# Kernel optimization log

Measured on AMD Instinct MI355X. Metric: run time of the kernel, lower is better.

Reference implementation:

```python
import jax, jax.numpy as jnp
import numpy as np

N_NODES = 100000
N_EDGES = 1600000
F_IN = 128
HID = 64
EPS = 1e-5


def setup_inputs() -> dict:
    key = jax.random.key(0)
    ks = jax.random.split(key, 16)
    x = jax.random.normal(ks[0], (N_NODES, F_IN), dtype=jnp.float32)
    edge_index = jax.random.randint(ks[1], (2, N_EDGES), 0, N_NODES, dtype=jnp.int64)
    inp = {"x": x, "edge_index": edge_index}
    # GCN layers: layer 0 maps F_IN->HID, layers 1,2 map HID->HID
    dims = [(F_IN, HID), (HID, HID), (HID, HID)]
    for i, (fi, fo) in enumerate(dims):
        inp[f"W{i}"] = jax.random.normal(ks[2 + i], (fi, fo), dtype=jnp.float32) / np.sqrt(fi)
        inp[f"b{i}"] = jnp.zeros((fo,), dtype=jnp.float32)
        inp[f"g{i}"] = jnp.ones((fo,), dtype=jnp.float32)
        inp[f"bt{i}"] = jnp.zeros((fo,), dtype=jnp.float32)
    inp["lw1"] = jax.random.normal(ks[8], (HID, HID // 2), dtype=jnp.float32) / np.sqrt(HID)
    inp["lb1"] = jnp.zeros((HID // 2,), dtype=jnp.float32)
    inp["lw2"] = jax.random.normal(ks[9], (HID // 2, 1), dtype=jnp.float32) / np.sqrt(HID // 2)
    inp["lb2"] = jnp.zeros((1,), dtype=jnp.float32)
    return inp


def _gcn_norm(edge_index, n_nodes):
    # add self loops, symmetric normalization D^{-1/2}(A+I)D^{-1/2}
    loops = jnp.arange(n_nodes, dtype=edge_index.dtype)
    src = jnp.concatenate([edge_index[0], loops])
    dst = jnp.concatenate([edge_index[1], loops])
    deg = jax.ops.segment_sum(jnp.ones_like(dst, dtype=jnp.float32), dst, num_segments=n_nodes)
    dinv = jax.lax.rsqrt(deg)  # deg >= 1 thanks to self loops
    norm = dinv[src] * dinv[dst]  # [E+N]
    return src, dst, norm


def reference(x, edge_index, W0, b0, g0, bt0, W1, b1, g1, bt1, W2, b2, g2, bt2, lw1, lb1, lw2, lb2):
    n = x.shape[0]
    src, dst, norm = _gcn_norm(edge_index, n)
    layers = [(W0, b0, g0, bt0), (W1, b1, g1, bt1), (W2, b2, g2, bt2)]
    h = x
    for W, b, g, bt in layers:
        hw = h @ W                                  # [N, H] dense GEMM
        msg = hw[src] * norm[:, None]               # gather + scale, [E+N, H]
        agg = jax.ops.segment_sum(msg, dst, num_segments=n) + b  # scatter-add
        # BatchNorm1d (training-mode batch stats, biased var)
        mu = agg.mean(axis=0)
        var = agg.var(axis=0)
        h = (agg - mu) * jax.lax.rsqrt(var + EPS) * g + bt
        h = jax.nn.relu(h)                          # dropout = identity (inference)
    h = jax.nn.relu(h @ lw1 + lb1)
    out = h @ lw2 + lb2                             # [N, 1]
    return out[:, 0]
```

## Files before the change

kernel.cpp:

```cpp
#include <hip/hip_runtime.h>
#include <hip/hip_fp16.h>

#define HIDW 64
#define EPSV 1e-5f
#define CAP 32
#define GRP 512
#define CHUNK 4096
#define PSLOTS 40
#define NBIN_MAX 256
#define NCHUNK_MAX 512
#define NSLOT 64
#define OVFR 32768

__global__ __launch_bounds__(256) void k_zero(int* __restrict__ deg, int* __restrict__ ovfcnt,
                                              float* __restrict__ stats, int n) {
    int i = blockIdx.x * 256 + threadIdx.x;
    if (i < n) deg[i] = 0;
    if (i < 2) ovfcnt[i] = 0;
    if (i < 3 * NSLOT * 128) stats[i] = 0.f;
}

__global__ __launch_bounds__(256) void k_part(const int* __restrict__ srcv, const int* __restrict__ dstv,
                                              int2* __restrict__ pairs, unsigned char* __restrict__ cnts,
                                              int2* __restrict__ ovfl, int* __restrict__ ovfcnt,
                                              int e, int nchunk, int nbin) {
    __shared__ int lcnt[NBIN_MAX];
    int tid = threadIdx.x;
    int chunk = blockIdx.x;
    for (int i = tid; i < nbin; i += 256) lcnt[i] = 0;
    __syncthreads();
    int base = chunk * CHUNK;
#pragma unroll
    for (int t = 0; t < CHUNK / 256; ++t) {
        int i = base + t * 256 + tid;
        if (i < e) {
            int s = srcv[i];
            int d = dstv[i];
            int k = d >> 9;
            int slot = atomicAdd(&lcnt[k], 1);
            if (slot < PSLOTS) {
                pairs[((size_t)k * nchunk + chunk) * PSLOTS + slot] = make_int2(s, d);
            } else {
                int o = atomicAdd(&ovfcnt[0], 1);
                if (o < OVFR) ovfl[o] = make_int2(s, d);
            }
        }
    }
    __syncthreads();
    for (int i = tid; i < nbin; i += 256)
        cnts[(size_t)i * nchunk + chunk] = (unsigned char)min(lcnt[i], PSLOTS);
}

__global__ __launch_bounds__(256) void k_own(const int2* __restrict__ pairs, const unsigned char* __restrict__ cnts,
                                             int* __restrict__ deg, unsigned char* __restrict__ bcnt,
                                             int* __restrict__ csr, int2* __restrict__ ovfl,
                                             int* __restrict__ ovfcnt, int n, int nchunk) {
    __shared__ int lcnt[GRP];
    __shared__ int bkt[GRP * CAP];
    __shared__ unsigned char scnt[NCHUNK_MAX];
    int g = blockIdx.x;
    int tid = threadIdx.x;
    int nbase = g << 9;
    int nloc = min(GRP, n - nbase);
    for (int i = tid; i < GRP; i += 256) lcnt[i] = 0;
    for (int i = tid; i < nchunk; i += 256) scnt[i] = cnts[(size_t)g * nchunk + i];
    __syncthreads();
    const int2* pb = pairs + (size_t)g * nchunk * PSLOTS;
    int tot = nchunk * PSLOTS;
    for (int i = tid; i < tot; i += 256) {
        int c = i / PSLOTS;
        int s = i - c * PSLOTS;
        if (s < (int)scnt[c]) {
            int2 p = pb[i];
            int loc = p.y - nbase;
            int pos = atomicAdd(&lcnt[loc], 1);
            if (pos < CAP) {
                bkt[loc * CAP + pos] = p.x;
            } else {
                int o = atomicAdd(&ovfcnt[1], 1);
                if (o < OVFR) ovfl[OVFR + o] = p;
            }
        }
    }
    __syncthreads();
    int* csrb = csr + (size_t)nbase * CAP;
    for (int i = tid; i < nloc * CAP; i += 256) csrb[i] = bkt[i];
    for (int i = tid; i < nloc; i += 256) {
        int c = lcnt[i];
        deg[nbase + i] = c;
        bcnt[nbase + i] = (unsigned char)min(c, CAP);
    }
}

__global__ __launch_bounds__(256) void k_ovfdeg(const int2* __restrict__ ovfl, const int* __restrict__ ovfcnt,
                                                int* __restrict__ deg) {
    int m0 = min(ovfcnt[0], OVFR);
    for (int i = threadIdx.x; i < m0; i += 256) atomicAdd(&deg[ovfl[i].y], 1);
}

__global__ __launch_bounds__(256) void k_ovf(const __half* __restrict__ hw, const int2* __restrict__ ovfl,
                                             const int* __restrict__ ovfcnt, const int* __restrict__ deg,
                                             float* __restrict__ agg) {
    int m0 = min(ovfcnt[0], OVFR);
    int m1 = min(ovfcnt[1], OVFR);
    int tot = m0 + m1;
    if (tot == 0) return;
    int lane = threadIdx.x & 63;
    int w = (blockIdx.x * 256 + threadIdx.x) >> 6;
    for (; w < tot; w += gridDim.x * 4) {
        int2 p = (w < m0) ? ovfl[w] : ovfl[OVFR + (w - m0)];
        float wt = rsqrtf(1.0f + (float)deg[p.y]);
        atomicAdd(&agg[(size_t)p.y * HIDW + lane], __half2float(hw[(size_t)p.x * HIDW + lane]) * wt);
    }
}

__global__ __launch_bounds__(256) void k_count(const int* __restrict__ dstv, int* __restrict__ deg, int e) {
    int i = blockIdx.x * 256 + threadIdx.x;
    if (i < e) atomicAdd(&deg[dstv[i]], 1);
}

__global__ __launch_bounds__(256) void k_scan1(const int* __restrict__ deg, int* __restrict__ off,
                                               int* __restrict__ bsum, int n) {
    __shared__ int s[256];
    int tid = threadIdx.x;
    int i = blockIdx.x * 256 + tid;
    int v = (i < n) ? deg[i] : 0;
    s[tid] = v;
    __syncthreads();
    for (int o = 1; o < 256; o <<= 1) {
        int t = (tid >= o) ? s[tid - o] : 0;
        __syncthreads();
        s[tid] += t;
        __syncthreads();
    }
    if (i < n) off[i] = s[tid] - v;
    if (tid == 255) bsum[blockIdx.x] = s[255];
}

__global__ __launch_bounds__(512) void k_scan2(int* __restrict__ bsum, int nb) {
    __shared__ int s[512];
    int tid = threadIdx.x;
    int v = (tid < nb) ? bsum[tid] : 0;
    s[tid] = v;
    __syncthreads();
    for (int o = 1; o < 512; o <<= 1) {
        int t = (tid >= o) ? s[tid - o] : 0;
        __syncthreads();
        s[tid] += t;
        __syncthreads();
    }
    if (tid < nb) bsum[tid] = s[tid] - v;
}

__global__ __launch_bounds__(256) void k_scan3(int* __restrict__ off, const int* __restrict__ bsum, int n) {
    int i = blockIdx.x * 256 + threadIdx.x;
    if (i < n) off[i] += bsum[blockIdx.x];
}

__global__ __launch_bounds__(256) void k_fill2(const int* __restrict__ srcv, const int* __restrict__ dstv,
                                               int* __restrict__ roff, int* __restrict__ csr, int e) {
    int i = blockIdx.x * 256 + threadIdx.x;
    if (i < e) {
        int d = dstv[i];
        int p = atomicAdd(&roff[d], 1);
        csr[p] = srcv[i];
    }
}

template <int K, bool BN>
__global__ __launch_bounds__(256) void k_gemm(const float* __restrict__ h, const float* __restrict__ W,
                                              __half* __restrict__ hw, int n,
                                              const float* __restrict__ st, const float* __restrict__ g,
                                              const float* __restrict__ bt, float invn,
                                              const int* __restrict__ deg) {
    constexpr int KP = K + 4;
    constexpr int KQ = K / 4;
    __shared__ float sH[64 * KP];
    __shared__ float sW[K * 64];
    __shared__ float sM[128];
    __shared__ float sSc[HIDW];
    __shared__ float sSh[HIDW];
    int tid = threadIdx.x;
    int node0 = blockIdx.x * 64;

    if (BN) {
        if (tid < 128) {
            float t = 0.f;
#pragma unroll 8
            for (int s = 0; s < NSLOT; ++s) t += st[s * 128 + tid];
            sM[tid] = t;
        }
        __syncthreads();
        if (tid < HIDW) {
            float mu = sM[tid] * invn;
            float var = sM[HIDW + tid] * invn - mu * mu;
            var = fmaxf(var, 0.f);
            float rstd = rsqrtf(var + EPSV);
            float sc = rstd * g[tid];
            sSc[tid] = sc;
            sSh[tid] = bt[tid] - mu * sc;
        }
        __syncthreads();
    }

    for (int i = tid; i < K * 16; i += 256)
        ((float4*)sW)[i] = ((const float4*)W)[i];
    for (int i = tid; i < 64 * KQ; i += 256) {
        int row = i / KQ, kq = i % KQ;
        int nn = node0 + row;
        if (nn >= n) nn = n - 1;
        float4 v = ((const float4*)h)[(size_t)nn * KQ + kq];
        if (BN) {
            int c = 4 * kq;
            v.x = fmaxf(fmaf(v.x, sSc[c + 0], sSh[c + 0]), 0.f);
            v.y = fmaxf(fmaf(v.y, sSc[c + 1], sSh[c + 1]), 0.f);
            v.z = fmaxf(fmaf(v.z, sSc[c + 2], sSh[c + 2]), 0.f);
            v.w = fmaxf(fmaf(v.w, sSc[c + 3], sSh[c + 3]), 0.f);
        }
        ((float4*)(sH + row * KP))[kq] = v;
    }
    __syncthreads();

    int tx = tid & 15;
    int ny = tid >> 4;
    const float* hbase = sH + (4 * ny) * KP;

    float acc[4][4];
#pragma unroll
    for (int j = 0; j < 4; ++j)
#pragma unroll
        for (int c = 0; c < 4; ++c) acc[j][c] = 0.f;

#pragma unroll 2
    for (int kq = 0; kq < KQ; ++kq) {
        float4 w0 = ((const float4*)(sW + (4 * kq + 0) * 64))[tx];
        float4 w1 = ((const float4*)(sW + (4 * kq + 1) * 64))[tx];
        float4 w2 = ((const float4*)(sW + (4 * kq + 2) * 64))[tx];
        float4 w3 = ((const float4*)(sW + (4 * kq + 3) * 64))[tx];
#pragma unroll
        for (int j = 0; j < 4; ++j) {
            float4 hv = ((const float4*)(hbase + j * KP))[kq];
            acc[j][0] = fmaf(hv.x, w0.x, acc[j][0]);
            acc[j][1] = fmaf(hv.x, w0.y, acc[j][1]);
            acc[j][2] = fmaf(hv.x, w0.z, acc[j][2]);
            acc[j][3] = fmaf(hv.x, w0.w, acc[j][3]);
            acc[j][0] = fmaf(hv.y, w1.x, acc[j][0]);
            acc[j][1] = fmaf(hv.y, w1.y, acc[j][1]);
            acc[j][2] = fmaf(hv.y, w1.z, acc[j][2]);
            acc[j][3] = fmaf(hv.y, w1.w, acc[j][3]);
            acc[j][0] = fmaf(hv.z, w2.x, acc[j][0]);
            acc[j][1] = fmaf(hv.z, w2.y, acc[j][1]);
            acc[j][2] = fmaf(hv.z, w2.z, acc[j][2]);
            acc[j][3] = fmaf(hv.z, w2.w, acc[j][3]);
            acc[j][0] = fmaf(hv.w, w3.x, acc[j][0]);
            acc[j][1] = fmaf(hv.w, w3.y, acc[j][1]);
            acc[j][2] = fmaf(hv.w, w3.z, acc[j][2]);
            acc[j][3] = fmaf(hv.w, w3.w, acc[j][3]);
        }
    }

#pragma unroll
    for (int j = 0; j < 4; ++j) {
        int node = node0 + 4 * ny + j;
        if (node < n) {
            float dv = rsqrtf(1.0f + (float)deg[node]);
            __half2 p01 = __floats2half2_rn(acc[j][0] * dv, acc[j][1] * dv);
            __half2 p23 = __floats2half2_rn(acc[j][2] * dv, acc[j][3] * dv);
            uint2 r;
            r.x = *(unsigned int*)&p01;
            r.y = *(unsigned int*)&p23;
            ((uint2*)hw)[(size_t)node * 16 + tx] = r;
        }
    }
}

__global__ __launch_bounds__(256) void k_gath8(const __half* __restrict__ hw, const int* __restrict__ csr,
                                               const int* __restrict__ deg, const unsigned char* __restrict__ bcnt,
                                               const float* __restrict__ bias,
                                               float* __restrict__ agg, float* __restrict__ st, int n) {
    __shared__ float sS[4 * 64];
    __shared__ float sQ[4 * 64];
    int tid = threadIdx.x;
    int lane = tid & 63;
    int w = tid >> 6;
    int g = lane >> 3;
    int p = lane & 7;
    int v = (blockIdx.x * 4 + w) * 8 + g;
    bool valid = (v < n);
    int vv = valid ? v : 0;
    int dcnt = deg[vv];
    int cnt = valid ? (int)bcnt[vv] : 0;
    float dv = rsqrtf(1.0f + (float)dcnt);
    const int* base = csr + (size_t)vv * CAP;
    const char* hwb = (const char*)hw;

    uint4 iv = ((const uint4*)base)[p];

    float4 b0 = ((const float4*)bias)[p * 2 + 0];
    float4 b1 = ((const float4*)bias)[p * 2 + 1];

    float acc[8];
    {
        uint4 sv = make_uint4(0, 0, 0, 0);
        if (valid) sv = *(const uint4*)(hwb + (((unsigned)vv << 7) + (p << 4)));
        const __half2* hp = (const __half2*)&sv;
#pragma unroll
        for (int i = 0; i < 4; ++i) {
            float2 f = __half22float2(hp[i]);
            acc[2 * i + 0] = f.x;
            acc[2 * i + 1] = f.y;
        }
    }

    int mc = cnt;
    mc = max(mc, __shfl_xor(mc, 8));
    mc = max(mc, __shfl_xor(mc, 16));
    mc = max(mc, __shfl_xor(mc, 32));

    int gl = lane & 56;
    for (int j0 = 0; j0 < mc; j0 += 8) {
        int sl = gl + (j0 >> 2);
        int idxs[8];
#pragma unroll
        for (int u = 0; u < 8; ++u) {
            int comp = u & 3;
            int word = (comp == 0) ? iv.x : (comp == 1) ? iv.y : (comp == 2) ? iv.z : iv.w;
            idxs[u] = __shfl(word, sl + (u >> 2));
        }
        uint4 rr[8];
#pragma unroll
        for (int u = 0; u < 8; ++u) {
            rr[u] = make_uint4(0, 0, 0, 0);
            if (j0 + u < cnt)
                rr[u] = *(const uint4*)(hwb + (((unsigned)idxs[u] << 7) + (p << 4)));
        }
#pragma unroll
        for (int u = 0; u < 8; ++u) {
            const __half2* hx = (const __half2*)&rr[u];
#pragma unroll
            for (int i = 0; i < 4; ++i) {
                float2 f = __half22float2(hx[i]);
                acc[2 * i + 0] += f.x;
                acc[2 * i + 1] += f.y;
            }
        }
    }

    float fin[8];
    fin[0] = fmaf(dv, acc[0], b0.x);
    fin[1] = fmaf(dv, acc[1], b0.y);
    fin[2] = fmaf(dv, acc[2], b0.z);
    fin[3] = fmaf(dv, acc[3], b0.w);
    fin[4] = fmaf(dv, acc[4], b1.x);
    fin[5] = fmaf(dv, acc[5], b1.y);
    fin[6] = fmaf(dv, acc[6], b1.z);
    fin[7] = fmaf(dv, acc[7], b1.w);
    if (valid) {
        float4 o0 = make_float4(fin[0], fin[1], fin[2], fin[3]);
        float4 o1 = make_float4(fin[4], fin[5], fin[6], fin[7]);
        float4* ap = (float4*)(agg + (size_t)vv * HIDW + p * 8);
        ap[0] = o0;
        ap[1] = o1;
    }
    float sv2[8], qv2[8];
#pragma unroll
    for (int i = 0; i < 8; ++i) {
        float t = valid ? fin[i] : 0.f;
        sv2[i] = t;
        qv2[i] = t * t;
    }
#pragma unroll
    for (int i = 0; i < 8; ++i) {
        sv2[i] += __shfl_xor(sv2[i], 8);
        qv2[i] += __shfl_xor(qv2[i], 8);
        sv2[i] += __shfl_xor(sv2[i], 16);
        qv2[i] += __shfl_xor(qv2[i], 16);
        sv2[i] += __shfl_xor(sv2[i], 32);
        qv2[i] += __shfl_xor(qv2[i], 32);
    }
    if (g == 0) {
#pragma unroll
        for (int i = 0; i < 8; ++i) {
            sS[w * 64 + p * 8 + i] = sv2[i];
            sQ[w * 64 + p * 8 + i] = qv2[i];
        }
    }
    __syncthreads();
    if (tid < 64) {
        float S = sS[tid] + sS[64 + tid] + sS[128 + tid] + sS[192 + tid];
        float Q = sQ[tid] + sQ[64 + tid] + sQ[128 + tid] + sQ[192 + tid];
        float* slot = st + (size_t)(blockIdx.x & (NSLOT - 1)) * 128;
        atomicAdd(&slot[tid], S);
        atomicAdd(&slot[64 + tid], Q);
    }
}

__global__ __launch_bounds__(256) void k_gatherB(const __half* __restrict__ hw, const int* __restrict__ csr,
                                                 const int* __restrict__ roff, const int* __restrict__ deg,
                                                 const float* __restrict__ bias,
                                                 float* __restrict__ agg, float* __restrict__ st, int n) {
    __shared__ float sS[4 * 64];
    __shared__ float sQ[4 * 64];
    int tid = threadIdx.x;
    int lane = tid & 63;
    int w = tid >> 6;
    int eh = lane >> 3;
    int c8 = lane & 7;
    int v = blockIdx.x * 4 + w;
    bool valid = (v < n);
    int vv = valid ? v : 0;
    int dcnt = deg[vv];
    float dv = rsqrtf(1.0f + (float)dcnt);
    int cnt = dcnt;
    const int* base = csr + (roff[vv] - dcnt);
    const char* hwb = (const char*)hw;

    float acc[8];
    {
        unsigned off0 = ((unsigned)vv << 7) + (c8 << 4);
        uint4 sv = *(const uint4*)(hwb + off0);
        const __half2* hp = (const __half2*)&sv;
#pragma unroll
        for (int i = 0; i < 4; ++i) {
            float2 f = __half22float2(hp[i]);
            acc[2 * i + 0] = (eh == 0) ? f.x : 0.f;
            acc[2 * i + 1] = (eh == 0) ? f.y : 0.f;
        }
    }

    for (int j0 = 0; j0 < cnt; j0 += 64) {
        int m = min(cnt - j0, 64);
        int idx = (lane < m) ? base[j0 + lane] : 0;
        int k = 0;
        for (; k + 16 <= m; k += 16) {
            int a0 = __shfl(idx, k + eh);
            int a1 = __shfl(idx, k + 8 + eh);
            uint4 v0 = *(const uint4*)(hwb + (((unsigned)a0 << 7) + (c8 << 4)));
            uint4 v1 = *(const uint4*)(hwb + (((unsigned)a1 << 7) + (c8 << 4)));
            const __half2* h0 = (const __half2*)&v0;
            const __half2* h1 = (const __half2*)&v1;
#pragma unroll
            for (int i = 0; i < 4; ++i) {
                float2 f0 = __half22float2(h0[i]);
                float2 f1 = __half22float2(h1[i]);
                acc[2 * i + 0] += f0.x + f1.x;
                acc[2 * i + 1] += f0.y + f1.y;
            }
        }
        for (; k < m; k += 8) {
            int a = __shfl(idx, k + eh);
            uint4 v0 = *(const uint4*)(hwb + (((unsigned)a << 7) + (c8 << 4)));
            if (k + eh < m) {
                const __half2* h0 = (const __half2*)&v0;
#pragma unroll
                for (int i = 0; i < 4; ++i) {
                    float2 f0 = __half22float2(h0[i]);
                    acc[2 * i + 0] += f0.x;
                    acc[2 * i + 1] += f0.y;
                }
            }
        }
    }
#pragma unroll
    for (int i = 0; i < 8; ++i) {
        acc[i] += __shfl_xor(acc[i], 8);
        acc[i] += __shfl_xor(acc[i], 16);
        acc[i] += __shfl_xor(acc[i], 32);
    }
    if (eh == 0) {
        float4 b0 = ((const float4*)bias)[c8 * 2 + 0];
        float4 b1 = ((const float4*)bias)[c8 * 2 + 1];
        float4 f0, f1;
        f0.x = fmaf(dv, acc[0], b0.x);
        f0.y = fmaf(dv, acc[1], b0.y);
        f0.z = fmaf(dv, acc[2], b0.z);
        f0.w = fmaf(dv, acc[3], b0.w);
        f1.x = fmaf(dv, acc[4], b1.x);
        f1.y = fmaf(dv, acc[5], b1.y);
        f1.z = fmaf(dv, acc[6], b1.z);
        f1.w = fmaf(dv, acc[7], b1.w);
        if (valid) {
            ((float4*)agg)[(size_t)vv * 16 + c8 * 2 + 0] = f0;
            ((float4*)agg)[(size_t)vv * 16 + c8 * 2 + 1] = f1;
        }
        float s0[8] = {f0.x, f0.y, f0.z, f0.w, f1.x, f1.y, f1.z, f1.w};
#pragma unroll
        for (int i = 0; i < 8; ++i) {
            float sv2 = valid ? s0[i] : 0.f;
            sS[w * 64 + c8 * 8 + i] = sv2;
            sQ[w * 64 + c8 * 8 + i] = sv2 * sv2;
        }
    }
    __syncthreads();
    if (tid < 64) {
        float S = sS[tid] + sS[64 + tid] + sS[128 + tid] + sS[192 + tid];
        float Q = sQ[tid] + sQ[64 + tid] + sQ[128 + tid] + sQ[192 + tid];
        float* slot = st + (size_t)(blockIdx.x & (NSLOT - 1)) * 128;
        atomicAdd(&slot[tid], S);
        atomicAdd(&slot[64 + tid], Q);
    }
}

__global__ __launch_bounds__(256) void k_head(const float* __restrict__ h, const float* __restrict__ lw1,
                                              const float* __restrict__ lb1, const float* __restrict__ lw2,
                                              const float* __restrict__ lb2, float* __restrict__ out, int n,
                                              const float* __restrict__ st, const float* __restrict__ g,
                                              const float* __restrict__ bt, float invn) {
    __shared__ float sW[64 * 32];
    __shared__ float sb1[32];
    __shared__ float sw2[32];
    __shared__ float sM[128];
    __shared__ float sSc[HIDW];
    __shared__ float sSh[HIDW];
    int tid = threadIdx.x;
    for (int i = tid; i < 64 * 32; i += 256) sW[i] = lw1[i];
    if (tid < 32) {
        sb1[tid] = lb1[tid];
        sw2[tid] = lw2[tid];
    }
    if (tid < 128) {
        float t = 0.f;
#pragma unroll 8
        for (int s = 0; s < NSLOT; ++s) t += st[s * 128 + tid];
        sM[tid] = t;
    }
    __syncthreads();
    if (tid < HIDW) {
        float mu = sM[tid] * invn;
        float var = sM[HIDW + tid] * invn - mu * mu;
        var = fmaxf(var, 0.f);
        float rstd = rsqrtf(var + EPSV);
        float sc = rstd * g[tid];
        sSc[tid] = sc;
        sSh[tid] = bt[tid] - mu * sc;
    }
    __syncthreads();
    int nd = blockIdx.x * 256 + tid;
    if (nd >= n) return;
    float acc[32];
#pragma unroll
    for (int j = 0; j < 32; ++j) acc[j] = sb1[j];
    const float4* hr = (const float4*)(h + (size_t)nd * HIDW);
#pragma unroll 4
    for (int kc = 0; kc < 16; ++kc) {
        float4 h4 = hr[kc];
        int c = 4 * kc;
        h4.x = fmaxf(fmaf(h4.x, sSc[c + 0], sSh[c + 0]), 0.f);
        h4.y = fmaxf(fmaf(h4.y, sSc[c + 1], sSh[c + 1]), 0.f);
        h4.z = fmaxf(fmaf(h4.z, sSc[c + 2], sSh[c + 2]), 0.f);
        h4.w = fmaxf(fmaf(h4.w, sSc[c + 3], sSh[c + 3]), 0.f);
        const float* w0 = &sW[(c + 0) * 32];
        const float* w1 = &sW[(c + 1) * 32];
        const float* w2 = &sW[(c + 2) * 32];
        const float* w3 = &sW[(c + 3) * 32];
#pragma unroll
        for (int j = 0; j < 32; ++j) {
            float t = fmaf(h4.x, w0[j], fmaf(h4.y, w1[j], fmaf(h4.z, w2[j], h4.w * w3[j])));
            acc[j] += t;
        }
    }
    float o = lb2[0];
#pragma unroll
    for (int j = 0; j < 32; ++j) o = fmaf(fmaxf(acc[j], 0.f), sw2[j], o);
    out[nd] = o;
}

extern "C" void kernel_launch(void* const* d_in, const int* in_sizes, int n_in,
                              void* d_out, int out_size, void* d_ws, size_t ws_size,
                              hipStream_t stream) {
    const float* x = (const float*)d_in[0];
    const int* ei = (const int*)d_in[1];
    const float* W[3] = {(const float*)d_in[2], (const float*)d_in[6], (const float*)d_in[10]};
    const float* B[3] = {(const float*)d_in[3], (const float*)d_in[7], (const float*)d_in[11]};
    const float* G[3] = {(const float*)d_in[4], (const float*)d_in[8], (const float*)d_in[12]};
    const float* BT[3] = {(const float*)d_in[5], (const float*)d_in[9], (const float*)d_in[13]};
    const float* lw1 = (const float*)d_in[14];
    const float* lb1 = (const float*)d_in[15];
    const float* lw2 = (const float*)d_in[16];
    const float* lb2 = (const float*)d_in[17];
    float* out = (float*)d_out;

    const int n = in_sizes[0] / 128;
    const int e = in_sizes[1] / 2;
    const int* srcv = ei;
    const int* dstv = ei + e;
    const float invn = 1.0f / (float)n;
    const int nchunk = (e + CHUNK - 1) / CHUNK;
    const int nbin = (n + GRP - 1) / GRP;

    char* ws = (char*)d_ws;
    size_t off = 0;
    auto alloc = [&](size_t bytes) -> char* {
        off = (off + 511) & ~(size_t)511;
        char* p = ws + off;
        off += bytes;
        return p;
    };
    float* stats = (float*)alloc((size_t)3 * NSLOT * 128 * 4);
    int* ovfcnt = (int*)alloc(512);
    int2* ovfl = (int2*)alloc((size_t)2 * OVFR * 8);
    unsigned char* cnts = (unsigned char*)alloc((size_t)nbin * nchunk);
    unsigned char* bcnt = (unsigned char*)alloc((size_t)n);
    int* deg = (int*)alloc((size_t)n * 4);
    float* bufA = (float*)alloc((size_t)n * HIDW * 4);
    __half* bufB = (__half*)alloc((size_t)n * HIDW * 2);
    size_t commonOff = off;

    size_t needA = ((commonOff + 511) & ~(size_t)511) + (size_t)n * CAP * 4;
    size_t pairsBytes = (size_t)nbin * nchunk * PSLOTS * 8;
    bool useA = (needA <= ws_size) && (pairsBytes <= (size_t)n * HIDW * 4) &&
                (nchunk <= NCHUNK_MAX) && (nbin <= NBIN_MAX);

    const int gN = (n + 255) / 256;
    const int gG = (n + 63) / 64;
    const int gV = (n + 3) / 4;
    const int gV8 = (n + 31) / 32;

    int2* pairs = (int2*)bufA;
    int* csrB = nullptr;
    int* roff = nullptr;
    int* bsum = nullptr;
    int* csrC = nullptr;

    if (useA) {
        csrB = (int*)alloc((size_t)n * CAP * 4);
        k_zero<<<gN, 256, 0, stream>>>(deg, ovfcnt, stats, n);
        k_part<<<nchunk, 256, 0, stream>>>(srcv, dstv, pairs, cnts, ovfl, ovfcnt, e, nchunk, nbin);
        k_own<<<nbin, 256, 0, stream>>>(pairs, cnts, deg, bcnt, csrB, ovfl, ovfcnt, n, nchunk);
        k_ovfdeg<<<1, 256, 0, stream>>>(ovfl, ovfcnt, deg);
    } else {
        roff = (int*)alloc((size_t)(n + 1) * 4);
        bsum = (int*)alloc(512 * 4);
        csrC = (int*)alloc((size_t)e * 4);
        k_zero<<<gN, 256, 0, stream>>>(deg, ovfcnt, stats, n);
        k_count<<<(e + 255) / 256, 256, 0, stream>>>(dstv, deg, e);
        k_scan1<<<gN, 256, 0, stream>>>(deg, roff, bsum, n);
        k_scan2<<<1, 512, 0, stream>>>(bsum, gN);
        k_scan3<<<gN, 256, 0, stream>>>(roff, bsum, n);
        k_fill2<<<(e + 255) / 256, 256, 0, stream>>>(srcv, dstv, roff, csrC, e);
    }

    for (int L = 0; L < 3; ++L) {
        float* stL = stats + (size_t)L * NSLOT * 128;
        if (L == 0)
            k_gemm<128, false><<<gG, 256, 0, stream>>>(x, W[0], bufB, n, nullptr, nullptr, nullptr, invn, deg);
        else
            k_gemm<64, true><<<gG, 256, 0, stream>>>(bufA, W[L], bufB, n, stats + (size_t)(L - 1) * NSLOT * 128,
                                                     G[L - 1], BT[L - 1], invn, deg);
        if (useA) {
            k_gath8<<<gV8, 256, 0, stream>>>(bufB, csrB, deg, bcnt, B[L], bufA, stL, n);
            k_ovf<<<16, 256, 0, stream>>>(bufB, ovfl, ovfcnt, deg, bufA);
        } else {
            k_gatherB<<<gV, 256, 0, stream>>>(bufB, csrC, roff, deg, B[L], bufA, stL, n);
        }
    }

    k_head<<<gN, 256, 0, stream>>>(bufA, lw1, lb1, lw2, lb2, out, n, stats + (size_t)2 * NSLOT * 128,
                                   G[2], BT[2], invn);
}
```

Baseline: 363.2 us.

## Retile dense GEMM to 256-node blocks with 8x8 register tiles and K-chunked transposed smem

Rewrites the node-feature GEMM so each block handles 256 nodes, and each thread computes an 8x8 output tile. The input is staged in 16-wide K chunks into a transposed shared buffer. This raises the FMA-to-LDS-load ratio and cuts the grid to a quarter of its former size, with wider 16-byte half-precision stores. In exchange, register pressure rises from 64 accumulators per thread, and there are fewer blocks and more syncs per K chunk.

```diff
diff --git a/kernel.cpp b/kernel.cpp
--- a/kernel.cpp
+++ b/kernel.cpp
@@ -173,15 +173,19 @@
                                               const float* __restrict__ st, const float* __restrict__ g,
                                               const float* __restrict__ bt, float invn,
                                               const int* __restrict__ deg) {
-    constexpr int KP = K + 4;
+    constexpr int KC = 16;
+    constexpr int NCH = K / KC;
     constexpr int KQ = K / 4;
-    __shared__ float sH[64 * KP];
+    constexpr int PT = 260;
     __shared__ float sW[K * 64];
+    __shared__ float sHT[KC][PT];
     __shared__ float sM[128];
     __shared__ float sSc[HIDW];
     __shared__ float sSh[HIDW];
     int tid = threadIdx.x;
-    int node0 = blockIdx.x * 64;
+    int tx = tid & 7;
+    int ty = tid >> 3;
+    int node0 = blockIdx.x * 256;
 
     if (BN) {
         if (tid < 128) {
@@ -200,76 +204,74 @@
             sSc[tid] = sc;
             sSh[tid] = bt[tid] - mu * sc;
         }
-        __syncthreads();
     }
 
     for (int i = tid; i < K * 16; i += 256)
         ((float4*)sW)[i] = ((const float4*)W)[i];
-    for (int i = tid; i < 64 * KQ; i += 256) {
-        int row = i / KQ, kq = i % KQ;
-        int nn = node0 + row;
-        if (nn >= n) nn = n - 1;
-        float4 v = ((const float4*)h)[(size_t)nn * KQ + kq];
-        if (BN) {
-            int c = 4 * kq;
-            v.x = fmaxf(fmaf(v.x, sSc[c + 0], sSh[c + 0]), 0.f);
-            v.y = fmaxf(fmaf(v.y, sSc[c + 1], sSh[c + 1]), 0.f);
-            v.z = fmaxf(fmaf(v.z, sSc[c + 2], sSh[c + 2]), 0.f);
-            v.w = fmaxf(fmaf(v.w, sSc[c + 3], sSh[c + 3]), 0.f);
-        }
-        ((float4*)(sH + row * KP))[kq] = v;
-    }
-    __syncthreads();
-
-    int tx = tid & 15;
-    int ny = tid >> 4;
-    const float* hbase = sH + (4 * ny) * KP;
-
-    float acc[4][4];
-#pragma unroll
-    for (int j = 0; j < 4; ++j)
-#pragma unroll
-        for (int c = 0; c < 4; ++c) acc[j][c] = 0.f;
-
-#pragma unroll 2
-    for (int kq = 0; kq < KQ; ++kq) {
-        float4 w0 = ((const float4*)(sW + (4 * kq + 0) * 64))[tx];
-        float4 w1 = ((const float4*)(sW + (4 * kq + 1) * 64))[tx];
-        float4 w2 = ((const float4*)(sW + (4 * kq + 2) * 64))[tx];
-        float4 w3 = ((const float4*)(sW + (4 * kq + 3) * 64))[tx];
-#pragma unroll
-        for (int j = 0; j < 4; ++j) {
-            float4 hv = ((const float4*)(hbase + j * KP))[kq];
-            acc[j][0] = fmaf(hv.x, w0.x, acc[j][0]);
-            acc[j][1] = fmaf(hv.x, w0.y, acc[j][1]);
-            acc[j][2] = fmaf(hv.x, w0.z, acc[j][2]);
-            acc[j][3] = fmaf(hv.x, w0.w, acc[j][3]);
-            acc[j][0] = fmaf(hv.y, w1.x, acc[j][0]);
-            acc[j][1] = fmaf(hv.y, w1.y, acc[j][1]);
-            acc[j][2] = fmaf(hv.y, w1.z, acc[j][2]);
-            acc[j][3] = fmaf(hv.y, w1.w, acc[j][3]);
-            acc[j][0] = fmaf(hv.z, w2.x, acc[j][0]);
-            acc[j][1] = fmaf(hv.z, w2.y, acc[j][1]);
-            acc[j][2] = fmaf(hv.z, w2.z, acc[j][2]);
-            acc[j][3] = fmaf(hv.z, w2.w, acc[j][3]);
-            acc[j][0] = fmaf(hv.w, w3.x, acc[j][0]);
-            acc[j][1] = fmaf(hv.w, w3.y, acc[j][1]);
-            acc[j][2] = fmaf(hv.w, w3.z, acc[j][2]);
-            acc[j][3] = fmaf(hv.w, w3.w, acc[j][3]);
-        }
-    }
-
-#pragma unroll
-    for (int j = 0; j < 4; ++j) {
-        int node = node0 + 4 * ny + j;
+
+    float acc[8][8];
+#pragma unroll
+    for (int j = 0; j < 8; ++j)
+#pragma unroll
+        for (int c = 0; c < 8; ++c) acc[j][c] = 0.f;
+
+#pragma unroll 1
+    for (int ch = 0; ch < NCH; ++ch) {
+        int kc0 = ch * KC;
+        __syncthreads();
+#pragma unroll
+        for (int it = 0; it < 4; ++it) {
+            int i = it * 256 + tid;
+            int node = i >> 2;
+            int q = i & 3;
+            int nn = node0 + node;
+            if (nn >= n) nn = n - 1;
+            float4 v = ((const float4*)h)[(size_t)nn * KQ + (kc0 >> 2) + q];
+            if (BN) {
+                int c = kc0 + 4 * q;
+                v.x = fmaxf(fmaf(v.x, sSc[c + 0], sSh[c + 0]), 0.f);
+                v.y = fmaxf(fmaf(v.y, sSc[c + 1], sSh[c + 1]), 0.f);
+                v.z = fmaxf(fmaf(v.z, sSc[c + 2], sSh[c + 2]), 0.f);
+                v.w = fmaxf(fmaf(v.w, sSc[c + 3], sSh[c + 3]), 0.f);
+            }
+            sHT[4 * q + 0][node] = v.x;
+            sHT[4 * q + 1][node] = v.y;
+            sHT[4 * q + 2][node] = v.z;
+            sHT[4 * q + 3][node] = v.w;
+        }
+        __syncthreads();
+#pragma unroll 4
+        for (int kk = 0; kk < KC; ++kk) {
+            float4 ha = *(const float4*)&sHT[kk][ty * 8];
+            float4 hb = *(const float4*)&sHT[kk][ty * 8 + 4];
+            const float* wr = sW + (kc0 + kk) * 64 + tx * 8;
+            float4 wa = *(const float4*)wr;
+            float4 wb = *(const float4*)(wr + 4);
+            float hv[8] = {ha.x, ha.y, ha.z, ha.w, hb.x, hb.y, hb.z, hb.w};
+            float wv[8] = {wa.x, wa.y, wa.z, wa.w, wb.x, wb.y, wb.z, wb.w};
+#pragma unroll
+            for (int j = 0; j < 8; ++j)
+#pragma unroll
+                for (int c = 0; c < 8; ++c)
+                    acc[j][c] = fmaf(hv[j], wv[c], acc[j][c]);
+        }
+    }
+
+#pragma unroll
+    for (int j = 0; j < 8; ++j) {
+        int node = node0 + ty * 8 + j;
         if (node < n) {
             float dv = rsqrtf(1.0f + (float)deg[node]);
-            __half2 p01 = __floats2half2_rn(acc[j][0] * dv, acc[j][1] * dv);
-            __half2 p23 = __floats2half2_rn(acc[j][2] * dv, acc[j][3] * dv);
-            uint2 r;
-            r.x = *(unsigned int*)&p01;
-            r.y = *(unsigned int*)&p23;
-            ((uint2*)hw)[(size_t)node * 16 + tx] = r;
+            __half2 p0 = __floats2half2_rn(acc[j][0] * dv, acc[j][1] * dv);
+            __half2 p1 = __floats2half2_rn(acc[j][2] * dv, acc[j][3] * dv);
+            __half2 p2 = __floats2half2_rn(acc[j][4] * dv, acc[j][5] * dv);
+            __half2 p3 = __floats2half2_rn(acc[j][6] * dv, acc[j][7] * dv);
+            uint4 r;
+            r.x = *(unsigned int*)&p0;
+            r.y = *(unsigned int*)&p1;
+            r.z = *(unsigned int*)&p2;
+            r.w = *(unsigned int*)&p3;
+            ((uint4*)hw)[(size_t)node * 8 + tx] = r;
         }
     }
 }
@@ -612,7 +614,7 @@
                 (nchunk <= NCHUNK_MAX) && (nbin <= NBIN_MAX);
 
     const int gN = (n + 255) / 256;
-    const int gG = (n + 63) / 64;
+    const int gG = (n + 255) / 256;
     const int gV = (n + 3) / 4;
     const int gV8 = (n + 31) / 32;
 
```

After: 364.2 us. Within noise of the previous version (+0.3%).
